# Performance work log

Hardware: AMD Instinct MI355X
Metric: run time of the kernel (lower is better)

## Reference

```python
import jax, jax.numpy as jnp
import numpy as np


def gcn_conv(h, W, b, src, dst):
    # PyG GCNConv: h @ W, add self-loops, symmetric deg^-1/2 normalization,
    # scatter-add messages from src to dst, then add bias.
    n = h.shape[0]
    h = h @ W                                   # [N, out]
    loop = jnp.arange(n, dtype=src.dtype)
    row = jnp.concatenate([src, loop])          # message sources
    col = jnp.concatenate([dst, loop])          # aggregation targets
    deg = jax.ops.segment_sum(jnp.ones_like(col, dtype=h.dtype), col, num_segments=n)
    dinv = jnp.where(deg > 0, jax.lax.rsqrt(deg), 0.0)
    norm = dinv[row] * dinv[col]                # [E+N]
    out = jax.ops.segment_sum(h[row] * norm[:, None], col, num_segments=n)
    return out + b


def setup_inputs() -> dict:
    key = jax.random.key(0)
    ks = jax.random.split(key, 12)
    N, E = 50000, 800000
    in_dim, hid, out_dim = 768, 256, 128
    x = jax.random.normal(ks[0], (N, in_dim), dtype=jnp.float32)
    edge_index = jax.random.randint(ks[1], (2, E), 0, N, dtype=jnp.int64)

    def lin(k, fan_in, fan_out):
        bound = 1.0 / np.sqrt(fan_in)
        kw, kb = jax.random.split(k)
        W = jax.random.uniform(kw, (fan_in, fan_out), jnp.float32, -bound, bound)
        b = jax.random.uniform(kb, (fan_out,), jnp.float32, -bound, bound)
        return W, b

    W1, b1 = lin(ks[2], in_dim, hid)
    Wg1, bg1 = lin(ks[3], hid, hid)
    Wg2, bg2 = lin(ks[4], hid, hid)
    W2, b2 = lin(ks[5], hid, out_dim)
    Wc, bc = lin(ks[6], out_dim, 2)
    return {
        "x": x, "edge_index": edge_index,
        "W1": W1, "b1": b1, "Wg1": Wg1, "bg1": bg1,
        "Wg2": Wg2, "bg2": bg2, "W2": W2, "b2": b2,
        "Wc": Wc, "bc": bc, "batch_size": 1024,
    }


def reference(x, edge_index, W1, b1, Wg1, bg1, Wg2, bg2, W2, b2, Wc, bc, batch_size):
    src, dst = edge_index[0], edge_index[1]
    h = jax.nn.relu(x @ W1 + b1)                # linear_relu1
    h = gcn_conv(h, Wg1, bg1, src, dst)         # text1
    # dropout is identity in eval mode
    h = gcn_conv(h, Wg2, bg2, src, dst)         # text2
    h = jax.nn.relu(h @ W2 + b2)                # linear_relu2
    logits = h @ Wc + bc                        # classifier
    return logits[:batch_size]
```

## Files before the change

### kernel.cpp

```cpp
#include <hip/hip_runtime.h>
#include <hip/hip_bf16.h>
#include <cstdint>
#include <cstddef>
#include <type_traits>

typedef _Float16 half8 __attribute__((ext_vector_type(8)));
typedef _Float16 half4v __attribute__((ext_vector_type(4)));
typedef float float4v __attribute__((ext_vector_type(4)));


__global__ void k_zero_int(int* __restrict__ p, int n) {
  int i = blockIdx.x * blockDim.x + threadIdx.x;
  if (i < n) p[i] = 0;
}

__global__ void k_count(const int* __restrict__ dst, int* __restrict__ cnt, int E) {
  int e = blockIdx.x * blockDim.x + threadIdx.x;
  if (e < E) atomicAdd(&cnt[dst[e]], 1);
}

__global__ __launch_bounds__(1024) void k_scan_local(const int* __restrict__ cnt,
                                                     int* __restrict__ rowp,
                                                     int* __restrict__ bsum, int n) {
  __shared__ int sm[1024];
  int tid = threadIdx.x;
  int i = blockIdx.x * 1024 + tid;
  int v = (i < n) ? cnt[i] : 0;
  sm[tid] = v;
  __syncthreads();
  for (int off = 1; off < 1024; off <<= 1) {
    int t = (tid >= off) ? sm[tid - off] : 0;
    __syncthreads();
    sm[tid] += t;
    __syncthreads();
  }
  if (i < n) rowp[i] = sm[tid] - v;
  if (tid == 1023) bsum[blockIdx.x] = sm[1023];
}

__global__ __launch_bounds__(1024) void k_scan_sums(int* __restrict__ bsum, int nb) {
  __shared__ int sm[1024];
  int tid = threadIdx.x;
  int v = (tid < nb) ? bsum[tid] : 0;
  sm[tid] = v;
  __syncthreads();
  for (int off = 1; off < 1024; off <<= 1) {
    int t = (tid >= off) ? sm[tid - off] : 0;
    __syncthreads();
    sm[tid] += t;
    __syncthreads();
  }
  if (tid < nb) bsum[tid] = sm[tid] - v;
}

__global__ void k_finalize(int* __restrict__ rowp, const int* __restrict__ bsum,
                           const int* __restrict__ cnt, int* __restrict__ cursor,
                           float* __restrict__ dinv, int n, int E) {
  int i = blockIdx.x * blockDim.x + threadIdx.x;
  if (i < n) {
    int v = rowp[i] + bsum[i >> 10];
    rowp[i] = v;
    cursor[i] = v;
    dinv[i] = rsqrtf((float)(cnt[i] + 1));
  }
  if (i == 0) rowp[n] = E;
}

__global__ void k_fill(const int* __restrict__ src, const int* __restrict__ dst,
                       int* __restrict__ cursor, int* __restrict__ csr_src, int E) {
  int e = blockIdx.x * blockDim.x + threadIdx.x;
  if (e < E) {
    int pos = atomicAdd(&cursor[dst[e]], 1);
    csr_src[pos] = src[e];
  }
}


__global__ void k_w_convert_all(const float* __restrict__ W1, const float* __restrict__ Wg1,
                                const float* __restrict__ Wg2, _Float16* __restrict__ W1t,
                                _Float16* __restrict__ Wg1t, _Float16* __restrict__ Wg2t,
                                int in_dim, int hid) {
  int idx = blockIdx.x * blockDim.x + threadIdx.x;
  int n1 = in_dim * hid;
  int n2 = hid * hid;
  if (idx < n1) {
    int n = idx / in_dim, k = idx - n * in_dim;
    W1t[idx] = (_Float16)W1[(size_t)k * hid + n];
  } else if (idx < n1 + n2) {
    int i2 = idx - n1;
    int n = i2 / hid, k = i2 - n * hid;
    Wg1t[i2] = (_Float16)Wg1[(size_t)k * hid + n];
  } else if (idx < n1 + 2 * n2) {
    int i2 = idx - n1 - n2;
    int n = i2 / hid, k = i2 - n * hid;
    Wg2t[i2] = (_Float16)Wg2[(size_t)k * hid + n];
  }
}


#define LDSS 40

template <typename AT>
__device__ __forceinline__ half8 load_row_h8(const AT* __restrict__ p, bool ok) {
  half8 v = {};
  if (ok) {
    if constexpr (std::is_same_v<AT, float>) {
      float4 f0 = *(const float4*)p;
      float4 f1 = *(const float4*)(p + 4);
      v[0] = (_Float16)f0.x; v[1] = (_Float16)f0.y;
      v[2] = (_Float16)f0.z; v[3] = (_Float16)f0.w;
      v[4] = (_Float16)f1.x; v[5] = (_Float16)f1.y;
      v[6] = (_Float16)f1.z; v[7] = (_Float16)f1.w;
    } else {
      v = *(const half8*)p;
    }
  }
  return v;
}

template <typename AT, int RELU, int BIAS, int SCALE>
__global__ __launch_bounds__(256, 4) void k_gemm_mfma(const AT* __restrict__ A,
                                                      const _Float16* __restrict__ Bt,
                                                      const float* __restrict__ bias,
                                                      const float* __restrict__ rowscale,
                                                      _Float16* __restrict__ out,
                                                      int M, int N, int K) {
  __shared__ _Float16 Asm[2][64 * LDSS];
  __shared__ _Float16 Bsm[2][128 * LDSS];
  const int tid = threadIdx.x;
  const int bm = blockIdx.y * 64;
  const int bn = blockIdx.x * 128;
  const int wave = tid >> 6;
  const int wm = (wave >> 1) * 32;
  const int wn = (wave & 1) * 64;
  const int quad = (tid & 63) >> 4;
  const int l15 = tid & 15;

  const int ar = tid >> 2;
  const int ac = (tid & 3) * 8;
  const int br0 = tid >> 1;

  const int gra = bm + ar;
  const bool oka = gra < M;
  const AT* Apt = A + (size_t)gra * K + ac;
  const int br_0 = tid >> 2, bc_0 = (tid & 3) * 8;
  const int br_1 = (tid + 256) >> 2, bc_1 = ((tid + 256) & 3) * 8;
  const _Float16* Bp0 = Bt + (size_t)(bn + br_0) * K + bc_0;
  const _Float16* Bp1 = Bt + (size_t)(bn + br_1) * K + bc_1;

  _Float16* AsW = &Asm[0][0] + ar * LDSS + ac;
  _Float16* BsW0 = &Bsm[0][0] + br_0 * LDSS + bc_0;
  _Float16* BsW1 = &Bsm[0][0] + br_1 * LDSS + bc_1;
  const int abufstep = 64 * LDSS;
  const int bbufstep = 128 * LDSS;
  (void)br0;

  float4v acc[2][4];
#pragma unroll
  for (int i = 0; i < 2; ++i)
#pragma unroll
    for (int j = 0; j < 4; ++j) acc[i][j] = (float4v){0.f, 0.f, 0.f, 0.f};

  half8 pa = load_row_h8<AT>(Apt, oka);
  half8 pb0 = *(const half8*)Bp0;
  half8 pb1 = *(const half8*)Bp1;
  *(half8*)AsW = pa;
  *(half8*)BsW0 = pb0;
  *(half8*)BsW1 = pb1;

  const int nk = K >> 5;
  int buf = 0;
  for (int kt = 0; kt < nk; ++kt) {
    __syncthreads();
    if (kt + 1 < nk) {
      int k0 = (kt + 1) << 5;
      pa = load_row_h8<AT>(Apt + k0, oka);
      pb0 = *(const half8*)(Bp0 + k0);
      pb1 = *(const half8*)(Bp1 + k0);
    }
    const _Float16* Ab = &Asm[0][0] + buf * abufstep;
    const _Float16* Bb = &Bsm[0][0] + buf * bbufstep;
    half8 af[2], bf[4];
#pragma unroll
    for (int i = 0; i < 2; ++i)
      af[i] = *(const half8*)(Ab + (wm + i * 16 + l15) * LDSS + quad * 8);
#pragma unroll
    for (int j = 0; j < 4; ++j)
      bf[j] = *(const half8*)(Bb + (wn + j * 16 + l15) * LDSS + quad * 8);
#pragma unroll
    for (int i = 0; i < 2; ++i)
#pragma unroll
      for (int j = 0; j < 4; ++j)
        acc[i][j] = __builtin_amdgcn_mfma_f32_16x16x32_f16(af[i], bf[j], acc[i][j], 0, 0, 0);
    if (kt + 1 < nk) {
      int nbuf = buf ^ 1;
      *(half8*)(AsW + nbuf * abufstep) = pa;
      *(half8*)(BsW0 + nbuf * bbufstep) = pb0;
      *(half8*)(BsW1 + nbuf * bbufstep) = pb1;
    }
    buf ^= 1;
  }

#pragma unroll
  for (int j = 0; j < 4; ++j) {
    int c = bn + wn + j * 16 + l15;
    float bv = BIAS ? bias[c] : 0.f;
#pragma unroll
    for (int i = 0; i < 2; ++i) {
      int rbase = bm + wm + i * 16 + quad * 4;
      float4v a = acc[i][j];
#pragma unroll
      for (int reg = 0; reg < 4; ++reg) {
        int r = rbase + reg;
        if (r < M) {
          float v = a[reg] + bv;
          if (RELU) v = fmaxf(v, 0.f);
          if (SCALE) v *= rowscale[r];
          out[(size_t)r * N + c] = (_Float16)v;
        }
      }
    }
  }
}


template <int RELU, int BIAS>
__global__ __launch_bounds__(256) void k_gemm(const float* __restrict__ A,
                                              const float* __restrict__ B,
                                              const float* __restrict__ bias,
                                              float* __restrict__ C,
                                              int M, int N, int K) {
  __shared__ float As[16][68];
  __shared__ float Bs[16][68];
  const int bm = blockIdx.y * 64;
  const int bn = blockIdx.x * 64;
  const int tid = threadIdx.x;
  const int tr = (tid >> 4) << 2;
  const int tc = (tid & 15) << 2;
  const int lm  = tid >> 2;
  const int lk  = (tid & 3) << 2;
  const int lk2 = tid >> 4;
  const int ln  = (tid & 15) << 2;
  const bool arow_ok = (bm + lm) < M;
  const float* Aptr = A + (size_t)(bm + lm) * K + lk;
  const float* Bptr = B + (size_t)lk2 * N + bn + ln;
  float acc[4][4] = {};
  for (int k0 = 0; k0 < K; k0 += 16) {
    float4 a4 = make_float4(0.f, 0.f, 0.f, 0.f);
    if (arow_ok) a4 = *(const float4*)(Aptr + k0);
    float4 b4 = *(const float4*)(Bptr + (size_t)k0 * N);
    As[lk + 0][lm] = a4.x;
    As[lk + 1][lm] = a4.y;
    As[lk + 2][lm] = a4.z;
    As[lk + 3][lm] = a4.w;
    *(float4*)&Bs[lk2][ln] = b4;
    __syncthreads();
#pragma unroll
    for (int k = 0; k < 16; ++k) {
      float4 av = *(const float4*)&As[k][tr];
      float4 bv = *(const float4*)&Bs[k][tc];
      float a[4] = {av.x, av.y, av.z, av.w};
      float b[4] = {bv.x, bv.y, bv.z, bv.w};
#pragma unroll
      for (int i = 0; i < 4; ++i)
#pragma unroll
        for (int j = 0; j < 4; ++j) acc[i][j] += a[i] * b[j];
    }
    __syncthreads();
  }
  float bias_v[4] = {0.f, 0.f, 0.f, 0.f};
  if (BIAS) {
    float4 bb = *(const float4*)(bias + bn + tc);
    bias_v[0] = bb.x; bias_v[1] = bb.y; bias_v[2] = bb.z; bias_v[3] = bb.w;
  }
#pragma unroll
  for (int i = 0; i < 4; ++i) {
    int r = bm + tr + i;
    if (r < M) {
      float4 o;
      o.x = acc[i][0] + bias_v[0];
      o.y = acc[i][1] + bias_v[1];
      o.z = acc[i][2] + bias_v[2];
      o.w = acc[i][3] + bias_v[3];
      if (RELU) {
        o.x = fmaxf(o.x, 0.f); o.y = fmaxf(o.y, 0.f);
        o.z = fmaxf(o.z, 0.f); o.w = fmaxf(o.w, 0.f);
      }
      *(float4*)&C[(size_t)r * N + bn + tc] = o;
    }
  }
}


template <typename OT>
__global__ __launch_bounds__(256) void k_agg(const _Float16* __restrict__ t,
                                             const int* __restrict__ row_ptr,
                                             const int* __restrict__ csr_src,
                                             const float* __restrict__ dinv,
                                             const float* __restrict__ bias,
                                             OT* __restrict__ out, int n_nodes) {
  int w = (int)((blockIdx.x * 256 + threadIdx.x) >> 6);
  int lane = threadIdx.x & 63;
  if (w >= n_nodes) return;
  float di = dinv[w];
  half4v v = *(const half4v*)(t + (size_t)w * 256 + lane * 4);
  float ax = (float)v[0], ay = (float)v[1], az = (float)v[2], aw = (float)v[3];
  int e0 = row_ptr[w], e1 = row_ptr[w + 1];
  int e = e0;
  for (; e + 4 <= e1; e += 4) {
    int s0 = csr_src[e];
    int s1 = csr_src[e + 1];
    int s2 = csr_src[e + 2];
    int s3 = csr_src[e + 3];
    half4v u0 = *(const half4v*)(t + (size_t)s0 * 256 + lane * 4);
    half4v u1 = *(const half4v*)(t + (size_t)s1 * 256 + lane * 4);
    half4v u2 = *(const half4v*)(t + (size_t)s2 * 256 + lane * 4);
    half4v u3 = *(const half4v*)(t + (size_t)s3 * 256 + lane * 4);
    ax += (float)u0[0] + (float)u1[0] + (float)u2[0] + (float)u3[0];
    ay += (float)u0[1] + (float)u1[1] + (float)u2[1] + (float)u3[1];
    az += (float)u0[2] + (float)u1[2] + (float)u2[2] + (float)u3[2];
    aw += (float)u0[3] + (float)u1[3] + (float)u2[3] + (float)u3[3];
  }
  for (; e < e1; ++e) {
    int s = csr_src[e];
    half4v u = *(const half4v*)(t + (size_t)s * 256 + lane * 4);
    ax += (float)u[0]; ay += (float)u[1]; az += (float)u[2]; aw += (float)u[3];
  }
  const float4 b = ((const float4*)bias)[lane];
  if constexpr (std::is_same_v<OT, float>) {
    float4 o;
    o.x = ax * di + b.x; o.y = ay * di + b.y;
    o.z = az * di + b.z; o.w = aw * di + b.w;
    ((float4*)(out + (size_t)w * 256))[lane] = o;
  } else {
    half4v o;
    o[0] = (_Float16)(ax * di + b.x); o[1] = (_Float16)(ay * di + b.y);
    o[2] = (_Float16)(az * di + b.z); o[3] = (_Float16)(aw * di + b.w);
    *(half4v*)(out + (size_t)w * 256 + lane * 4) = o;
  }
}


__global__ __launch_bounds__(256) void k_cls(const float* __restrict__ h,
                                             const float* __restrict__ Wc,
                                             const float* __restrict__ bc,
                                             float* __restrict__ out, int M, int K) {
  __shared__ float w[512];
  for (int i = threadIdx.x; i < 2 * K; i += 256) w[i] = Wc[i];
  __syncthreads();
  int i = blockIdx.x * 256 + threadIdx.x;
  if (i >= M) return;
  float a0 = bc[0], a1 = bc[1];
  const float* hr = h + (size_t)i * K;
  for (int k = 0; k < K; ++k) {
    float a = hr[k];
    a0 += a * w[2 * k];
    a1 += a * w[2 * k + 1];
  }
  out[2 * i] = a0;
  out[2 * i + 1] = a1;
}


extern "C" void kernel_launch(void* const* d_in, const int* in_sizes, int n_in,
                              void* d_out, int out_size, void* d_ws, size_t ws_size,
                              hipStream_t stream) {
  const float* x   = (const float*)d_in[0];
  const int*   ei  = (const int*)d_in[1];
  const float* W1  = (const float*)d_in[2];
  const float* b1  = (const float*)d_in[3];
  const float* Wg1 = (const float*)d_in[4];
  const float* bg1 = (const float*)d_in[5];
  const float* Wg2 = (const float*)d_in[6];
  const float* bg2 = (const float*)d_in[7];
  const float* W2  = (const float*)d_in[8];
  const float* b2  = (const float*)d_in[9];
  const float* Wc  = (const float*)d_in[10];
  const float* bc  = (const float*)d_in[11];
  float* out = (float*)d_out;

  const int hid     = in_sizes[3];
  const int in_dim  = in_sizes[2] / hid;
  const int out_dim = in_sizes[9];
  const int N       = in_sizes[0] / in_dim;
  const int E       = in_sizes[1] / 2;
  const int Batch   = out_size / 2;

  const int* srcI = ei;
  const int* dstI = ei + E;

  char* ws = (char*)d_ws;
  size_t off = 0;
  auto alloc = [&](size_t bytes) -> void* {
    void* p = ws + off;
    off = (off + bytes + 255) & ~(size_t)255;
    return p;
  };
  _Float16* h0h  = (_Float16*)alloc((size_t)N * hid * 2);
  _Float16* t1h  = (_Float16*)alloc((size_t)N * hid * 2);
  _Float16* h1h  = (_Float16*)alloc((size_t)N * hid * 2);
  _Float16* t2h  = (_Float16*)alloc((size_t)N * hid * 2);
  _Float16* W1t  = (_Float16*)alloc((size_t)in_dim * hid * 2);
  _Float16* Wg1t = (_Float16*)alloc((size_t)hid * hid * 2);
  _Float16* Wg2t = (_Float16*)alloc((size_t)hid * hid * 2);
  float* agg2    = (float*)alloc((size_t)Batch * hid * 4);
  float* h3      = (float*)alloc((size_t)Batch * out_dim * 4);
  float* dinv    = (float*)alloc((size_t)N * 4);
  int*   cnt     = (int*)alloc((size_t)N * 4);
  int*   rowp    = (int*)alloc((size_t)(N + 1) * 4);
  int*   bsum    = (int*)alloc((size_t)1024 * 4);
  int*   cursor  = (int*)alloc((size_t)N * 4);
  int*   csrs    = (int*)alloc((size_t)E * 4);
  (void)ws_size; (void)n_in;

  dim3 blk(256);
  const int nb = (N + 1023) / 1024;

  k_zero_int<<<(N + 255) / 256, blk, 0, stream>>>(cnt, N);
  k_count<<<(E + 255) / 256, blk, 0, stream>>>(dstI, cnt, E);
  k_scan_local<<<nb, 1024, 0, stream>>>(cnt, rowp, bsum, N);
  k_scan_sums<<<1, 1024, 0, stream>>>(bsum, nb);
  k_finalize<<<(N + 255) / 256, blk, 0, stream>>>(rowp, bsum, cnt, cursor, dinv, N, E);
  k_fill<<<(E + 255) / 256, blk, 0, stream>>>(srcI, dstI, cursor, csrs, E);

  {
    int total = in_dim * hid + 2 * hid * hid;
    k_w_convert_all<<<(total + 255) / 256, blk, 0, stream>>>(W1, Wg1, Wg2, W1t, Wg1t, Wg2t, in_dim, hid);
  }

  dim3 gemm_grid(hid / 128, (N + 63) / 64);
  k_gemm_mfma<float, 1, 1, 0><<<gemm_grid, blk, 0, stream>>>(x, W1t, b1, nullptr, h0h, N, hid, in_dim);
  k_gemm_mfma<_Float16, 0, 0, 1><<<gemm_grid, blk, 0, stream>>>(h0h, Wg1t, nullptr, dinv, t1h, N, hid, hid);
  k_agg<_Float16><<<(N + 3) / 4, blk, 0, stream>>>(t1h, rowp, csrs, dinv, bg1, h1h, N);
  k_gemm_mfma<_Float16, 0, 0, 1><<<gemm_grid, blk, 0, stream>>>(h1h, Wg2t, nullptr, dinv, t2h, N, hid, hid);
  k_agg<float><<<(Batch + 3) / 4, blk, 0, stream>>>(t2h, rowp, csrs, dinv, bg2, agg2, Batch);
  k_gemm<1, 1><<<dim3(out_dim / 64, (Batch + 63) / 64), blk, 0, stream>>>(agg2, W2, b2, h3, Batch, out_dim, hid);
  k_cls<<<(Batch + 255) / 256, blk, 0, stream>>>(h3, Wc, bc, out, Batch, out_dim);
}
```

Before: 538.4 us.

## Restructure MFMA GEMM to register-resident A fragments with full-width N tile

Replaces the 64x128 double-buffered LDS GEMM with a kernel in which each block covers 128 rows and the full 256 output columns. A fragments are loaded straight from global memory into registers, and B is staged through LDS in K chunks of 128. Each A row is now read once instead of once per N-tile, and the K dimension is a template constant. The cost is a large accumulator (32 float4 per lane), lower occupancy (launch bound of 2), and no overlap between global loads and MFMA work across chunks.

```diff
diff --git a/kernel.cpp b/kernel.cpp
--- a/kernel.cpp
+++ b/kernel.cpp
@@ -98,10 +98,10 @@
 }
 
 
-#define LDSS 40
+#define BSTR 136
 
 template <typename AT>
-__device__ __forceinline__ half8 load_row_h8(const AT* __restrict__ p, bool ok) {
+__device__ __forceinline__ half8 load_a_h8(const AT* __restrict__ p, bool ok) {
   half8 v = {};
   if (ok) {
     if constexpr (std::is_same_v<AT, float>) {
@@ -118,105 +118,86 @@
   return v;
 }
 
-template <typename AT, int RELU, int BIAS, int SCALE>
-__global__ __launch_bounds__(256, 4) void k_gemm_mfma(const AT* __restrict__ A,
-                                                      const _Float16* __restrict__ Bt,
-                                                      const float* __restrict__ bias,
-                                                      const float* __restrict__ rowscale,
-                                                      _Float16* __restrict__ out,
-                                                      int M, int N, int K) {
-  __shared__ _Float16 Asm[2][64 * LDSS];
-  __shared__ _Float16 Bsm[2][128 * LDSS];
+template <typename AT, int K_, int RELU, int BIAS, int SCALE>
+__global__ __launch_bounds__(256, 2) void k_gemm_rs(const AT* __restrict__ A,
+                                                    const _Float16* __restrict__ Bt,
+                                                    const float* __restrict__ bias,
+                                                    const float* __restrict__ rowscale,
+                                                    _Float16* __restrict__ out, int M) {
+  constexpr int CK = 128;
+  constexpr int NCH = K_ / CK;
+  __shared__ _Float16 Bs[256 * BSTR];
+
   const int tid = threadIdx.x;
-  const int bm = blockIdx.y * 64;
-  const int bn = blockIdx.x * 128;
   const int wave = tid >> 6;
-  const int wm = (wave >> 1) * 32;
-  const int wn = (wave & 1) * 64;
-  const int quad = (tid & 63) >> 4;
-  const int l15 = tid & 15;
-
-  const int ar = tid >> 2;
-  const int ac = (tid & 3) * 8;
-  const int br0 = tid >> 1;
-
-  const int gra = bm + ar;
-  const bool oka = gra < M;
-  const AT* Apt = A + (size_t)gra * K + ac;
-  const int br_0 = tid >> 2, bc_0 = (tid & 3) * 8;
-  const int br_1 = (tid + 256) >> 2, bc_1 = ((tid + 256) & 3) * 8;
-  const _Float16* Bp0 = Bt + (size_t)(bn + br_0) * K + bc_0;
-  const _Float16* Bp1 = Bt + (size_t)(bn + br_1) * K + bc_1;
-
-  _Float16* AsW = &Asm[0][0] + ar * LDSS + ac;
-  _Float16* BsW0 = &Bsm[0][0] + br_0 * LDSS + bc_0;
-  _Float16* BsW1 = &Bsm[0][0] + br_1 * LDSS + bc_1;
-  const int abufstep = 64 * LDSS;
-  const int bbufstep = 128 * LDSS;
-  (void)br0;
-
-  float4v acc[2][4];
+  const int lane = tid & 63;
+  const int quad = lane >> 4;
+  const int l15 = lane & 15;
+  const int wrow = blockIdx.x * 128 + wave * 32;
+
+  const int r0 = wrow + l15, r1 = wrow + 16 + l15;
+  const bool ok0 = r0 < M, ok1 = r1 < M;
+  const AT* Ap0 = A + (size_t)r0 * K_ + quad * 8;
+  const AT* Ap1 = A + (size_t)r1 * K_ + quad * 8;
+
+  float4v acc[2][16];
 #pragma unroll
   for (int i = 0; i < 2; ++i)
 #pragma unroll
-    for (int j = 0; j < 4; ++j) acc[i][j] = (float4v){0.f, 0.f, 0.f, 0.f};
-
-  half8 pa = load_row_h8<AT>(Apt, oka);
-  half8 pb0 = *(const half8*)Bp0;
-  half8 pb1 = *(const half8*)Bp1;
-  *(half8*)AsW = pa;
-  *(half8*)BsW0 = pb0;
-  *(half8*)BsW1 = pb1;
-
-  const int nk = K >> 5;
-  int buf = 0;
-  for (int kt = 0; kt < nk; ++kt) {
-    __syncthreads();
-    if (kt + 1 < nk) {
-      int k0 = (kt + 1) << 5;
-      pa = load_row_h8<AT>(Apt + k0, oka);
-      pb0 = *(const half8*)(Bp0 + k0);
-      pb1 = *(const half8*)(Bp1 + k0);
-    }
-    const _Float16* Ab = &Asm[0][0] + buf * abufstep;
-    const _Float16* Bb = &Bsm[0][0] + buf * bbufstep;
-    half8 af[2], bf[4];
-#pragma unroll
-    for (int i = 0; i < 2; ++i)
-      af[i] = *(const half8*)(Ab + (wm + i * 16 + l15) * LDSS + quad * 8);
-#pragma unroll
-    for (int j = 0; j < 4; ++j)
-      bf[j] = *(const half8*)(Bb + (wn + j * 16 + l15) * LDSS + quad * 8);
-#pragma unroll
-    for (int i = 0; i < 2; ++i)
-#pragma unroll
-      for (int j = 0; j < 4; ++j)
-        acc[i][j] = __builtin_amdgcn_mfma_f32_16x16x32_f16(af[i], bf[j], acc[i][j], 0, 0, 0);
-    if (kt + 1 < nk) {
-      int nbuf = buf ^ 1;
-      *(half8*)(AsW + nbuf * abufstep) = pa;
-      *(half8*)(BsW0 + nbuf * bbufstep) = pb0;
-      *(half8*)(BsW1 + nbuf * bbufstep) = pb1;
-    }
-    buf ^= 1;
-  }
-
-#pragma unroll
-  for (int j = 0; j < 4; ++j) {
-    int c = bn + wn + j * 16 + l15;
+    for (int j = 0; j < 16; ++j) acc[i][j] = (float4v){0.f, 0.f, 0.f, 0.f};
+
+  for (int ck = 0; ck < NCH; ++ck) {
+    const int kbase = ck * CK;
+    half8 af0[4], af1[4];
+#pragma unroll
+    for (int s = 0; s < 4; ++s) {
+      af0[s] = load_a_h8<AT>(Ap0 + kbase + s * 32, ok0);
+      af1[s] = load_a_h8<AT>(Ap1 + kbase + s * 32, ok1);
+    }
+    __syncthreads();
+#pragma unroll
+    for (int it = 0; it < 16; ++it) {
+      int i = tid + it * 256;
+      int n = i >> 4, g = i & 15;
+      *(half8*)(Bs + n * BSTR + g * 8) =
+          *(const half8*)(Bt + (size_t)n * K_ + kbase + g * 8);
+    }
+    __syncthreads();
+#pragma unroll
+    for (int j = 0; j < 16; ++j) {
+#pragma unroll
+      for (int s = 0; s < 4; ++s) {
+        half8 bf = *(const half8*)(Bs + (j * 16 + l15) * BSTR + s * 32 + quad * 8);
+        acc[0][j] = __builtin_amdgcn_mfma_f32_16x16x32_f16(af0[s], bf, acc[0][j], 0, 0, 0);
+        acc[1][j] = __builtin_amdgcn_mfma_f32_16x16x32_f16(af1[s], bf, acc[1][j], 0, 0, 0);
+      }
+    }
+  }
+
+  float rs[2][4];
+#pragma unroll
+  for (int rg = 0; rg < 2; ++rg)
+#pragma unroll
+    for (int reg = 0; reg < 4; ++reg) {
+      int r = wrow + rg * 16 + quad * 4 + reg;
+      rs[rg][reg] = (SCALE && r < M) ? rowscale[r] : 1.f;
+    }
+#pragma unroll
+  for (int j = 0; j < 16; ++j) {
+    int c = j * 16 + l15;
     float bv = BIAS ? bias[c] : 0.f;
 #pragma unroll
-    for (int i = 0; i < 2; ++i) {
-      int rbase = bm + wm + i * 16 + quad * 4;
-      float4v a = acc[i][j];
+    for (int rg = 0; rg < 2; ++rg) {
+      int rbase = wrow + rg * 16 + quad * 4;
+      float4v a = acc[rg][j];
 #pragma unroll
       for (int reg = 0; reg < 4; ++reg) {
         int r = rbase + reg;
         if (r < M) {
           float v = a[reg] + bv;
           if (RELU) v = fmaxf(v, 0.f);
-          if (SCALE) v *= rowscale[r];
-          out[(size_t)r * N + c] = (_Float16)v;
+          if (SCALE) v *= rs[rg][reg];
+          out[(size_t)r * 256 + c] = (_Float16)v;
         }
       }
     }
@@ -428,11 +409,11 @@
     k_w_convert_all<<<(total + 255) / 256, blk, 0, stream>>>(W1, Wg1, Wg2, W1t, Wg1t, Wg2t, in_dim, hid);
   }
 
-  dim3 gemm_grid(hid / 128, (N + 63) / 64);
-  k_gemm_mfma<float, 1, 1, 0><<<gemm_grid, blk, 0, stream>>>(x, W1t, b1, nullptr, h0h, N, hid, in_dim);
-  k_gemm_mfma<_Float16, 0, 0, 1><<<gemm_grid, blk, 0, stream>>>(h0h, Wg1t, nullptr, dinv, t1h, N, hid, hid);
+  const int gblocks = (N + 127) / 128;
+  k_gemm_rs<float, 768, 1, 1, 0><<<gblocks, blk, 0, stream>>>(x, W1t, b1, nullptr, h0h, N);
+  k_gemm_rs<_Float16, 256, 0, 0, 1><<<gblocks, blk, 0, stream>>>(h0h, Wg1t, nullptr, dinv, t1h, N);
   k_agg<_Float16><<<(N + 3) / 4, blk, 0, stream>>>(t1h, rowp, csrs, dinv, bg1, h1h, N);
-  k_gemm_mfma<_Float16, 0, 0, 1><<<gemm_grid, blk, 0, stream>>>(h1h, Wg2t, nullptr, dinv, t2h, N, hid, hid);
+  k_gemm_rs<_Float16, 256, 0, 0, 1><<<gblocks, blk, 0, stream>>>(h1h, Wg2t, nullptr, dinv, t2h, N);
   k_agg<float><<<(Batch + 3) / 4, blk, 0, stream>>>(t2h, rowp, csrs, dinv, bg2, agg2, Batch);
   k_gemm<1, 1><<<dim3(out_dim / 64, (Batch + 63) / 64), blk, 0, stream>>>(agg2, W2, b2, h3, Batch, out_dim, hid);
   k_cls<<<(Batch + 255) / 256, blk, 0, stream>>>(h3, Wc, bc, out, Batch, out_dim);
```

Result: no change. 543.8 us (+1.0%).
